# Performance work log

Measured on AMD Instinct MI355X. Metric: run time of the kernel, lower is better.

The kernel has to match this reference:

```python
import jax, jax.numpy as jnp
import numpy as np

N = 32768   # 'a' nodes
K = 8       # incoming edges per node (regular graph)
K2 = K // 2
E = N * K   # edges, stored as reverse pairs (2i, 2i+1)
D = 300     # hid_dim
H = 4       # attention heads
DEPTH = 3


def _build_graph():
    i = np.arange(N)
    src = np.empty(E, np.int64)
    mail = np.empty((N, K), np.int64)
    for d in range(1, K2 + 1):
        base = 2 * (i * K2 + (d - 1))
        src[base] = i                 # edge i -> (i+d)%N
        src[base + 1] = (i + d) % N   # reverse edge (i+d)%N -> i
        # incoming edges of node v: ((v-d)->v) and ((v+d)->v)
        mail[:, 2 * (d - 1)] = 2 * (((i - d) % N) * K2 + (d - 1))
        mail[:, 2 * (d - 1) + 1] = 2 * (i * K2 + (d - 1)) + 1
    return src, mail


def setup_inputs() -> dict:
    key = jax.random.key(0)
    ks = jax.random.split(key, 12)
    s = 1.0 / np.sqrt(D)
    src, mail = _build_graph()
    return {
        'f': jax.random.normal(ks[0], (N, D), jnp.float32),
        'x': jax.random.normal(ks[1], (E, D), jnp.float32),
        'mail_idx': jnp.asarray(mail),
        'src_idx': jnp.asarray(src),
        'Wq': jax.random.normal(ks[2], (D, D), jnp.float32) * s,
        'bq': jnp.zeros((D,), jnp.float32),
        'Wk': jax.random.normal(ks[3], (D, D), jnp.float32) * s,
        'bk': jnp.zeros((D,), jnp.float32),
        'Wv': jax.random.normal(ks[4], (D, D), jnp.float32) * s,
        'bv': jnp.zeros((D,), jnp.float32),
        'Wo': jax.random.normal(ks[5], (D, D), jnp.float32) * s,
        'bo': jnp.zeros((D,), jnp.float32),
        'Wmp': jax.random.normal(ks[6], (DEPTH - 1, D, D), jnp.float32) * s,
        'bmp': jnp.zeros((DEPTH - 1, D), jnp.float32),
        'Wlast': jax.random.normal(ks[7], (3 * D, D), jnp.float32) * s,
        'blast': jnp.zeros((D,), jnp.float32),
    }


def _mha(q_in, k_in, v_in, Wq, bq, Wk, bk, Wv, bv, Wo, bo):
    # q_in: [N,1,D], k_in/v_in: [N,K,D]  (per-node neighborhood attention)
    dk = D // H
    q = (q_in @ Wq + bq).reshape(N, 1, H, dk).transpose(0, 2, 1, 3)
    k = (k_in @ Wk + bk).reshape(N, -1, H, dk).transpose(0, 2, 1, 3)
    v = (v_in @ Wv + bv).reshape(N, -1, H, dk).transpose(0, 2, 1, 3)
    scores = jnp.einsum('nhqd,nhkd->nhqk', q, k) / jnp.sqrt(jnp.float32(dk))
    p = jax.nn.softmax(scores, axis=-1)
    o = jnp.einsum('nhqk,nhkd->nhqd', p, v).transpose(0, 2, 1, 3).reshape(N, 1, D)
    return o @ Wo + bo


def reference(f, x, mail_idx, src_idx, Wq, bq, Wk, bk, Wv, bv, Wo, bo,
              Wmp, bmp, Wlast, blast):
    rev = jnp.arange(E) ^ 1  # reverse_edge: swap within consecutive pairs
    f_h = f              # init_node: f_h = f.clone()
    h = x                # init_edge: h = x.clone()
    for i in range(DEPTH - 1):
        mail = h[mail_idx]                    # copy_e mailbox [N,K,D]
        feat = f_h[:, None, :]                # [N,1,D]
        # add_attn: attn(feat, mail, mail + feat)
        f_h = _mha(feat, mail, mail + feat,
                   Wq, bq, Wk, bk, Wv, bv, Wo, bo)[:, 0, :]
        rev_h = h[rev]                        # paired reverse-edge feature
        m = f_h[src_idx] - rev_h              # del_reverse_message
        h = jax.nn.relu(x + m @ Wmp[i] + bmp[i])  # update_edge
    # final node update: Linear(cat([sum(mailbox h), f_h, f]))
    mail_sum = jnp.sum(h[mail_idx], axis=1)   # [N,D]
    f_final = jnp.concatenate([mail_sum, f_h, f], axis=1) @ Wlast + blast
    return f_final
```

## Files before the change

### kernel.cpp

```cpp
#include <hip/hip_runtime.h>

typedef unsigned short u16;
typedef unsigned int u32;
typedef __bf16 bf16x8 __attribute__((ext_vector_type(8)));
typedef float f32x4 __attribute__((ext_vector_type(4)));

#define N_NODES 32768
#define E_EDGES 262144
#define BQ_U16 26240
#define S75 0.11547005383792515f

__device__ __forceinline__ float b2f(u16 u) {
    union { u32 u; float f; } x; x.u = ((u32)u) << 16; return x.f;
}
__device__ __forceinline__ u16 f2b(float f) {
    union { float f; u32 u; } x; x.f = f;
    u32 r = x.u + 0x7FFF + ((x.u >> 16) & 1);
    return (u16)(r >> 16);
}
__device__ __forceinline__ u32 bsub2(u32 a, u32 b) {
    float lo = b2f((u16)(a & 0xFFFF)) - b2f((u16)(b & 0xFFFF));
    float hi = b2f((u16)(a >> 16))    - b2f((u16)(b >> 16));
    return (u32)f2b(lo) | ((u32)f2b(hi) << 16);
}

#define GLOAD16(g, l) \
    __builtin_amdgcn_global_load_lds((const __attribute__((address_space(1))) u32*)(g), \
                                     (__attribute__((address_space(3))) u32*)(l), 16, 0, 0)

__global__ void convT_k(const float* __restrict__ src, int R, int C,
                        u16* __restrict__ dst, int KP_, long total) {
    long id = (long)blockIdx.x * blockDim.x + threadIdx.x;
    if (id >= total) return;
    int n = (int)(id / KP_), k = (int)(id % KP_);
    dst[id] = (k < R && n < C) ? f2b(src[(long)k * C + n]) : (u16)0;
}

__global__ void convTq_k(const float* __restrict__ src, u16* __restrict__ dst) {
    int id = blockIdx.x * 256 + threadIdx.x;
    if (id >= 4 * BQ_U16) return;
    int q = id / BQ_U16, rem = id % BQ_U16;
    int r = rem / 328, c = rem % 328;
    int n = q * 80 + r;
    dst[id] = (c < 300 && n < 300) ? f2b(src[(long)c * 300 + n]) : (u16)0;
}

__global__ void wqkq_k(const float* __restrict__ Wq, const float* __restrict__ Wk,
                       u16* __restrict__ dst) {
    int id = blockIdx.x * 256 + threadIdx.x;
    if (id >= 16 * BQ_U16) return;
    int q = id / BQ_U16, rem = id % BQ_U16;
    int r = rem / 328, c = rem % 328;
    int h = q >> 2;
    int cc = (q & 3) * 80 + r;
    float acc = 0.f;
    if (c < 300 && cc < 300) {
        const float* wq = Wq + (long)c * 300 + 75 * h;
        const float* wk = Wk + (long)cc * 300 + 75 * h;
        for (int d = 0; d < 75; ++d) acc += wq[d] * wk[d];
        acc *= S75;
    }
    dst[id] = f2b(acc);
}

__global__ void bqk_k(const float* __restrict__ bq, const float* __restrict__ Wk,
                      float* __restrict__ dst) {
    int n = blockIdx.x * 256 + threadIdx.x;
    if (n >= 1280) return;
    int h = n / 320, cc = n % 320;
    float acc = 0.f;
    if (cc < 300) {
        const float* b = bq + 75 * h;
        const float* wk = Wk + (long)cc * 300 + 75 * h;
        for (int d = 0; d < 75; ++d) acc += b[d] * wk[d];
        acc *= S75;
    }
    dst[n] = acc;
}

__global__ void ucat_k(const float* __restrict__ Wv, const float* __restrict__ Wo,
                       u16* __restrict__ dst) {
    long id = (long)blockIdx.x * 256 + threadIdx.x;
    if (id >= 320L * 1600) return;
    int n = (int)(id / 1600), k = (int)(id % 1600);
    float acc = 0.f;
    if (n < 300) {
        if (k < 1280) {
            int h = k / 320, a = k % 320;
            if (a < 300) {
                const float* wv = Wv + (long)a * 300 + 75 * h;
                const float* wo = Wo + (long)(75 * h) * 300 + n;
                for (int d = 0; d < 75; ++d) acc += wv[d] * wo[(long)d * 300];
            }
        } else {
            int a = k - 1280;
            if (a < 300) {
                const float* wv = Wv + (long)a * 300;
                const float* wo = Wo + n;
                for (int d = 0; d < 300; ++d) acc += wv[d] * wo[(long)d * 300];
            }
        }
    }
    dst[id] = f2b(acc);
}

__global__ void bvo_k(const float* __restrict__ bv, const float* __restrict__ Wo,
                      const float* __restrict__ bo, float* __restrict__ dst) {
    int n = blockIdx.x * 256 + threadIdx.x;
    if (n >= 320) return;
    float acc = 0.f;
    if (n < 300) {
        for (int d = 0; d < 300; ++d) acc += bv[d] * Wo[(long)d * 300 + n];
        acc += bo[n];
    }
    dst[n] = acc;
}

__global__ void padconv_k(const float* __restrict__ src, int C,
                          u16* __restrict__ dst, int CP,
                          u16* __restrict__ dst2, int CP2, long total) {
    long id = (long)blockIdx.x * blockDim.x + threadIdx.x;
    if (id >= total) return;
    int cw = CP >> 3;
    long row = id / cw;
    int c8 = (int)(id % cw) * 8;
    u32 w[4];
    #pragma unroll
    for (int p = 0; p < 4; ++p) {
        int c0 = c8 + 2 * p, c1 = c0 + 1;
        u16 lo = (c0 < C) ? f2b(src[row * C + c0]) : (u16)0;
        u16 hi = (c1 < C) ? f2b(src[row * C + c1]) : (u16)0;
        w[p] = (u32)lo | ((u32)hi << 16);
    }
    u32* d = (u32*)(dst + row * CP + c8);
    d[0] = w[0]; d[1] = w[1]; d[2] = w[2]; d[3] = w[3];
    if (dst2) {
        u32* d2 = (u32*)(dst2 + row * CP2 + c8);
        d2[0] = w[0]; d2[1] = w[1]; d2[2] = w[2]; d2[3] = w[3];
    }
}

#define TCOMP(KB, APTR) do { \
    bf16x8 av_[2], bb_[5]; \
    _Pragma("unroll") for (int fr = 0; fr < 2; ++fr) \
        av_[fr] = *(const bf16x8*)&(APTR)[ar0 + fr * 512]; \
    _Pragma("unroll") for (int fc = 0; fc < 5; ++fc) \
        bb_[fc] = *(const bf16x8*)&Bs[br0 + fc * 5248 + (KB) * 32]; \
    __builtin_amdgcn_s_setprio(1); \
    _Pragma("unroll") for (int fr = 0; fr < 2; ++fr) \
        _Pragma("unroll") for (int fc = 0; fc < 5; ++fc) \
            acc[fr][fc] = __builtin_amdgcn_mfma_f32_16x16x32_bf16(bb_[fc], av_[fr], acc[fr][fc], 0, 0, 0); \
    __builtin_amdgcn_s_setprio(0); \
} while (0)

__global__ __launch_bounds__(256, 2) void qgemm_k(
    const u16* __restrict__ A, const u16* __restrict__ Bswz,
    const float* __restrict__ bias, u16* __restrict__ outB)
{
    __shared__ __attribute__((aligned(16))) u16 Bs[80 * 328];
    __shared__ __attribute__((aligned(16))) u16 As3[3][128 * 32];
    const int tid = threadIdx.x;
    const int wf = tid >> 6, lane = tid & 63;
    const int tl = lane & 15, thi = lane >> 4;
    const int bid = blockIdx.x;
    const int gid = (bid & 7) * ((int)gridDim.x >> 3) + (bid >> 3);
    const long m0 = (long)(gid >> 4) * 128;
    const int q = gid & 15;
    const int n0 = q * 80;
    const int wf_u = __builtin_amdgcn_readfirstlane(wf);
    const u16* Bsrc = Bswz + q * BQ_U16;

    #pragma unroll
    for (int i = 0; i < 13; ++i) {
        int t = i * 256 + tid;
        if (t < 3280)
            GLOAD16(Bsrc + (long)t * 8, &Bs[(i * 256 + wf_u * 64) * 8]);
    }
    const int r1 = tid >> 2;
    const int g1 = (tid & 3) ^ ((r1 >> 1) & 3);
    const u16* gA0 = A + (m0 + r1) * 320L + g1 * 8;
    const u16* gA1 = A + (m0 + 64 + r1) * 320L + g1 * 8;

#define ESTAGE(KB) { \
    GLOAD16(gA0 + (KB) * 32, &As3[(KB) % 3][wf_u * 512]); \
    GLOAD16(gA1 + (KB) * 32, &As3[(KB) % 3][2048 + wf_u * 512]); }

    ESTAGE(0); ESTAGE(1);

    f32x4 acc[2][5];
    #pragma unroll
    for (int i = 0; i < 2; ++i)
        #pragma unroll
        for (int j = 0; j < 5; ++j) acc[i][j] = (f32x4)(0.f);
    const int ar0 = (wf * 32 + tl) * 32 + (thi ^ ((tl >> 1) & 3)) * 8;
    const int br0 = tl * 328 + thi * 8;

#define ESTEP(KB, VN) { \
    asm volatile("s_waitcnt vmcnt(" #VN ")" ::: "memory"); \
    __builtin_amdgcn_s_barrier(); \
    __builtin_amdgcn_sched_barrier(0); \
    if ((KB) + 2 < 10) ESTAGE((KB) + 2); \
    TCOMP(KB, (&As3[(KB) % 3][0])); }

    ESTEP(0, 2) ESTEP(1, 2) ESTEP(2, 2) ESTEP(3, 2) ESTEP(4, 2)
    ESTEP(5, 2) ESTEP(6, 2) ESTEP(7, 2) ESTEP(8, 2) ESTEP(9, 0)
#undef ESTEP
#undef ESTAGE

    #pragma unroll
    for (int fr = 0; fr < 2; ++fr) {
        const long row = m0 + wf * 32 + fr * 16 + tl;
        #pragma unroll
        for (int fc = 0; fc < 5; ++fc) {
            const int c0 = n0 + fc * 16 + thi * 4;
            f32x4 v = acc[fr][fc];
            const float4 bs = *(const float4*)&bias[c0];
            v[0] += bs.x; v[1] += bs.y; v[2] += bs.z; v[3] += bs.w;
            uint2 p;
            p.x = (u32)f2b(v[0]) | ((u32)f2b(v[1]) << 16);
            p.y = (u32)f2b(v[2]) | ((u32)f2b(v[3]) << 16);
            *(uint2*)&outB[row * 1280 + c0] = p;
        }
    }
}

__global__ __launch_bounds__(256) void attn2_k(
    const u16* __restrict__ qg, const u16* __restrict__ hcur,
    const int* __restrict__ mail, u16* __restrict__ wideA)
{
    const int tid = threadIdx.x;
    const long n = (long)blockIdx.x * 4 + (tid >> 6);
    const int lane = tid & 63;
    const bool act = lane < 40;
    const int ll = act ? lane : 39;

    int idx[8];
    #pragma unroll
    for (int j = 0; j < 8; ++j) idx[j] = mail[n * 8 + j];
    uint4 hr[8];
    #pragma unroll
    for (int j = 0; j < 8; ++j)
        hr[j] = *(const uint4*)&hcur[(long)idx[j] * 320 + ll * 8];
    uint4 qv[4];
    #pragma unroll
    for (int h = 0; h < 4; ++h)
        qv[h] = *(const uint4*)&qg[n * 1280 + h * 320 + ll * 8];
    if (!act) {
        #pragma unroll
        for (int j = 0; j < 8; ++j) hr[j] = make_uint4(0, 0, 0, 0);
    }

    float qf[4][8];
    #pragma unroll
    for (int h = 0; h < 4; ++h) {
        const u32 w[4] = {qv[h].x, qv[h].y, qv[h].z, qv[h].w};
        #pragma unroll
        for (int p = 0; p < 4; ++p) {
            qf[h][2 * p]     = b2f((u16)(w[p] & 0xFFFF));
            qf[h][2 * p + 1] = b2f((u16)(w[p] >> 16));
        }
    }

    float s[4][8];
    #pragma unroll
    for (int j = 0; j < 8; ++j) {
        float hf[8];
        const u32 w[4] = {hr[j].x, hr[j].y, hr[j].z, hr[j].w};
        #pragma unroll
        for (int p = 0; p < 4; ++p) {
            hf[2 * p]     = b2f((u16)(w[p] & 0xFFFF));
            hf[2 * p + 1] = b2f((u16)(w[p] >> 16));
        }
        #pragma unroll
        for (int h = 0; h < 4; ++h) {
            float d = 0.f;
            #pragma unroll
            for (int m = 0; m < 8; ++m) d += qf[h][m] * hf[m];
            d += __shfl_xor(d, 32, 64);
            d += __shfl_xor(d, 16, 64);
            d += __shfl_xor(d, 8, 64);
            d += __shfl_xor(d, 4, 64);
            d += __shfl_xor(d, 2, 64);
            d += __shfl_xor(d, 1, 64);
            s[h][j] = d;
        }
    }

    float p_[4][8];
    #pragma unroll
    for (int h = 0; h < 4; ++h) {
        float mx = s[h][0];
        #pragma unroll
        for (int j = 1; j < 8; ++j) mx = fmaxf(mx, s[h][j]);
        float sum = 0.f;
        #pragma unroll
        for (int j = 0; j < 8; ++j) { p_[h][j] = __expf(s[h][j] - mx); sum += p_[h][j]; }
        const float inv = 1.f / sum;
        #pragma unroll
        for (int j = 0; j < 8; ++j) p_[h][j] *= inv;
    }

    float y[4][8];
    #pragma unroll
    for (int h = 0; h < 4; ++h)
        #pragma unroll
        for (int m = 0; m < 8; ++m) y[h][m] = 0.f;
    #pragma unroll
    for (int j = 0; j < 8; ++j) {
        float hf[8];
        const u32 w[4] = {hr[j].x, hr[j].y, hr[j].z, hr[j].w};
        #pragma unroll
        for (int p = 0; p < 4; ++p) {
            hf[2 * p]     = b2f((u16)(w[p] & 0xFFFF));
            hf[2 * p + 1] = b2f((u16)(w[p] >> 16));
        }
        #pragma unroll
        for (int h = 0; h < 4; ++h)
            #pragma unroll
            for (int m = 0; m < 8; ++m) y[h][m] += p_[h][j] * hf[m];
    }
    if (act) {
        #pragma unroll
        for (int h = 0; h < 4; ++h) {
            uint4 o;
            o.x = (u32)f2b(y[h][0]) | ((u32)f2b(y[h][1]) << 16);
            o.y = (u32)f2b(y[h][2]) | ((u32)f2b(y[h][3]) << 16);
            o.z = (u32)f2b(y[h][4]) | ((u32)f2b(y[h][5]) << 16);
            o.w = (u32)f2b(y[h][6]) | ((u32)f2b(y[h][7]) << 16);
            *(uint4*)&wideA[n * 1600 + h * 320 + lane * 8] = o;
        }
    }
}

__global__ __launch_bounds__(256, 2) void egemmmb_k(
    const u16* __restrict__ fhb, const u16* __restrict__ hcur,
    const u16* __restrict__ hx, const int* __restrict__ srcidx,
    const u16* __restrict__ Bswz, const float* __restrict__ bias,
    u16* __restrict__ outB)
{
    __shared__ __attribute__((aligned(16))) u16 Bs[80 * 328];
    __shared__ __attribute__((aligned(16))) u16 As2[2][128 * 32];
    const int tid = threadIdx.x;
    const int wf = tid >> 6, lane = tid & 63;
    const int tl = lane & 15, thi = lane >> 4;
    const int bid = blockIdx.x;
    const int gid = (bid & 7) * ((int)gridDim.x >> 3) + (bid >> 3);
    const long m0 = (long)(gid >> 2) * 128;
    const int q = gid & 3;
    const int n0 = q * 80;
    const int wf_u = __builtin_amdgcn_readfirstlane(wf);
    const u16* Bsrc = Bswz + q * BQ_U16;

    #pragma unroll
    for (int i = 0; i < 13; ++i) {
        int t = i * 256 + tid;
        if (t < 3280)
            GLOAD16(Bsrc + (long)t * 8, &Bs[(i * 256 + wf_u * 64) * 8]);
    }
    const int r1 = tid >> 2;
    const int g1 = (tid & 3) ^ ((r1 >> 1) & 3);
    const long e0 = m0 + r1, e1 = m0 + 64 + r1;
    const u16* pF0 = fhb + (long)srcidx[e0] * 320 + g1 * 8;
    const u16* pH0 = hcur + (e0 ^ 1) * 320 + g1 * 8;
    const u16* pF1 = fhb + (long)srcidx[e1] * 320 + g1 * 8;
    const u16* pH1 = hcur + (e1 ^ 1) * 320 + g1 * 8;

    uint4 Fa0, Ha0, Fa1, Ha1, Fb0, Hb0, Fb1, Hb1, Fc0, Hc0, Fc1, Hc1;

#define MLOAD(KB, F0, H0, F1, H1) { \
    F0 = *(const uint4*)(pF0 + (KB) * 32); H0 = *(const uint4*)(pH0 + (KB) * 32); \
    F1 = *(const uint4*)(pF1 + (KB) * 32); H1 = *(const uint4*)(pH1 + (KB) * 32); }

#define MWRITE(KB, F0, H0, F1, H1) { \
    u16* wb_ = &As2[(KB) & 1][0]; \
    uint4 o_; \
    o_.x = bsub2(F0.x, H0.x); o_.y = bsub2(F0.y, H0.y); \
    o_.z = bsub2(F0.z, H0.z); o_.w = bsub2(F0.w, H0.w); \
    *(uint4*)&wb_[tid * 8] = o_; \
    o_.x = bsub2(F1.x, H1.x); o_.y = bsub2(F1.y, H1.y); \
    o_.z = bsub2(F1.z, H1.z); o_.w = bsub2(F1.w, H1.w); \
    *(uint4*)&wb_[(tid + 256) * 8] = o_; }

    MLOAD(0, Fa0, Ha0, Fa1, Ha1);
    MLOAD(1, Fb0, Hb0, Fb1, Hb1);
    MLOAD(2, Fc0, Hc0, Fc1, Hc1);
    asm volatile("s_waitcnt vmcnt(8)" ::: "memory");
    MWRITE(0, Fa0, Ha0, Fa1, Ha1);

    f32x4 acc[2][5];
    #pragma unroll
    for (int i = 0; i < 2; ++i)
        #pragma unroll
        for (int j = 0; j < 5; ++j) acc[i][j] = (f32x4)(0.f);
    const int ar0 = (wf * 32 + tl) * 32 + (thi ^ ((tl >> 1) & 3)) * 8;
    const int br0 = tl * 328 + thi * 8;

#define MSTEP(KB, VN, LF0, LH0, LF1, LH1, SF0, SH0, SF1, SH1) { \
    if ((KB) + 3 < 10) MLOAD((KB) + 3, LF0, LH0, LF1, LH1); \
    asm volatile("s_waitcnt vmcnt(" #VN ")" ::: "memory"); \
    asm volatile("s_waitcnt lgkmcnt(0)" ::: "memory"); \
    __builtin_amdgcn_s_barrier(); \
    __builtin_amdgcn_sched_barrier(0); \
    if ((KB) + 1 < 10) MWRITE((KB) + 1, SF0, SH0, SF1, SH1); \
    TCOMP(KB, (&As2[(KB) & 1][0])); }

    MSTEP(0, 8, Fa0, Ha0, Fa1, Ha1, Fb0, Hb0, Fb1, Hb1)
    MSTEP(1, 8, Fb0, Hb0, Fb1, Hb1, Fc0, Hc0, Fc1, Hc1)
    MSTEP(2, 8, Fc0, Hc0, Fc1, Hc1, Fa0, Ha0, Fa1, Ha1)
    MSTEP(3, 8, Fa0, Ha0, Fa1, Ha1, Fb0, Hb0, Fb1, Hb1)
    MSTEP(4, 8, Fb0, Hb0, Fb1, Hb1, Fc0, Hc0, Fc1, Hc1)
    MSTEP(5, 8, Fc0, Hc0, Fc1, Hc1, Fa0, Ha0, Fa1, Ha1)
    MSTEP(6, 8, Fa0, Ha0, Fa1, Ha1, Fb0, Hb0, Fb1, Hb1)
    MSTEP(7, 4, Fb0, Hb0, Fb1, Hb1, Fc0, Hc0, Fc1, Hc1)
    MSTEP(8, 0, Fc0, Hc0, Fc1, Hc1, Fa0, Ha0, Fa1, Ha1)
    MSTEP(9, 0, Fa0, Ha0, Fa1, Ha1, Fb0, Hb0, Fb1, Hb1)
#undef MSTEP
#undef MLOAD
#undef MWRITE

    #pragma unroll
    for (int fr = 0; fr < 2; ++fr) {
        const long row = m0 + wf * 32 + fr * 16 + tl;
        #pragma unroll
        for (int fc = 0; fc < 5; ++fc) {
            const int c0 = n0 + fc * 16 + thi * 4;
            f32x4 v = acc[fr][fc];
            if (bias && c0 < 300) {
                const float4 bs = *(const float4*)&bias[c0];
                v[0] += bs.x; v[1] += bs.y; v[2] += bs.z; v[3] += bs.w;
            }
            {
                const ushort4 xv = *(const ushort4*)&hx[row * 320 + c0];
                v[0] += b2f(xv.x); v[1] += b2f(xv.y); v[2] += b2f(xv.z); v[3] += b2f(xv.w);
            }
            v[0] = fmaxf(v[0], 0.f); v[1] = fmaxf(v[1], 0.f);
            v[2] = fmaxf(v[2], 0.f); v[3] = fmaxf(v[3], 0.f);
            uint2 p;
            p.x = (u32)f2b(v[0]) | ((u32)f2b(v[1]) << 16);
            p.y = (u32)f2b(v[2]) | ((u32)f2b(v[3]) << 16);
            *(uint2*)&outB[row * 320 + c0] = p;
        }
    }
}

#define LOADB(bq, kt1) { const long ko_ = (long)(kt1) << 6; \
    _Pragma("unroll") for (int fc = 0; fc < 5; ++fc) \
      _Pragma("unroll") for (int ks = 0; ks < 2; ++ks) \
        bq[fc][ks] = *(const bf16x8*)(gBw + (long)fc * 16 * KP + ko_ + ks * 32); }

#define READA(lkt) { \
    _Pragma("unroll") for (int fr = 0; fr < 4; ++fr) \
      _Pragma("unroll") for (int ks = 0; ks < 2; ++ks) \
        a[fr][ks] = *(const bf16x8*)&As[(fr * 16 + tl) * 320 + ((((lkt) * 8 + ks * 4 + thi) ^ sx) * 8)]; }

#define DOMFMA(bq) { _Pragma("unroll") for (int fr = 0; fr < 4; ++fr) \
    _Pragma("unroll") for (int fc = 0; fc < 5; ++fc) \
      _Pragma("unroll") for (int ks = 0; ks < 2; ++ks) \
        acc[fr][fc] = __builtin_amdgcn_mfma_f32_16x16x32_bf16(bq[fc][ks], a[fr][ks], acc[fr][fc], 0, 0, 0); }

template<int KP>
__global__ __launch_bounds__(256, 2) void gemm_k(
    const u16* __restrict__ A,
    const u16* __restrict__ BT,
    const float* __restrict__ bias,
    float* __restrict__ outF, int ostride, int ocols,
    u16* __restrict__ outB1, long strideB1,
    u16* __restrict__ outB2, long strideB2)
{
    __shared__ u16 As[64 * 320];
    const int tid = threadIdx.x;
    const int w = tid >> 6, lane = tid & 63;
    const int tl = lane & 15, thi = lane >> 4;
    const int sx = tl & 7;
    const long m0 = (long)blockIdx.x * 64;
    const int w_u = __builtin_amdgcn_readfirstlane(w);

    const u16* gBw = BT + ((long)(w * 80 + tl)) * KP + thi * 8;

    f32x4 acc[4][5];
    #pragma unroll
    for (int i = 0; i < 4; ++i)
        #pragma unroll
        for (int j = 0; j < 5; ++j) acc[i][j] = (f32x4)(0.f);

    constexpr int NCH = KP / 320;
    constexpr int NST = KP >> 6;
    bf16x8 bA[5][2], bB[5][2], a[4][2];

    #pragma unroll
    for (int kb = 0; kb < NCH; ++kb) {
        if (kb) __syncthreads();
        #pragma unroll
        for (int i = 0; i < 10; ++i) {
            const int c = i * 256 + w_u * 64 + lane;
            const int r = c / 40, s = c - r * 40;
            GLOAD16(A + (m0 + r) * (long)KP + kb * 320 + ((s ^ (r & 7)) * 8),
                    &As[(i * 256 + w_u * 64) * 8]);
        }
        if (kb == 0) LOADB(bA, 0);
        __syncthreads();
        #pragma unroll
        for (int lkt = 0; lkt < 5; ++lkt) {
            const int kt = kb * 5 + lkt;
            if (kt + 1 < NST) {
                if (kt & 1) { LOADB(bA, kt + 1); } else { LOADB(bB, kt + 1); }
            }
            READA(lkt);
            if (kt & 1) { DOMFMA(bB); } else { DOMFMA(bA); }
        }
    }

    #pragma unroll
    for (int fr = 0; fr < 4; ++fr) {
        const long row = m0 + fr * 16 + tl;
        #pragma unroll
        for (int fc = 0; fc < 5; ++fc) {
            const int c0 = w * 80 + fc * 16 + thi * 4;
            f32x4 v = acc[fr][fc];
            if (bias && c0 < 300) {
                const float4 bs = *(const float4*)&bias[c0];
                v[0] += bs.x; v[1] += bs.y; v[2] += bs.z; v[3] += bs.w;
            }
            if (outF && c0 < ocols)
                *(float4*)&outF[row * (long)ostride + c0] = make_float4(v[0], v[1], v[2], v[3]);
            if (outB1 || outB2) {
                uint2 p;
                p.x = (u32)f2b(v[0]) | ((u32)f2b(v[1]) << 16);
                p.y = (u32)f2b(v[2]) | ((u32)f2b(v[3]) << 16);
                if (outB1) *(uint2*)&outB1[row * strideB1 + c0] = p;
                if (outB2) *(uint2*)&outB2[row * strideB2 + c0] = p;
            }
        }
    }
}

__global__ __launch_bounds__(256) void concat_k(
    const u16* __restrict__ hb, const u16* __restrict__ fhb,
    const float* __restrict__ f, const int* __restrict__ mail,
    u16* __restrict__ Acat)
{
    const long n = blockIdx.x;
    int m[8];
    #pragma unroll
    for (int j = 0; j < 8; ++j) m[j] = mail[n * 8 + j];
    for (int c = threadIdx.x; c < 960; c += 256) {
        float v;
        if (c < 300) {
            float s = 0.f;
            #pragma unroll
            for (int j = 0; j < 8; ++j) s += b2f(hb[(long)m[j] * 320 + c]);
            v = s;
        } else if (c < 600) v = b2f(fhb[n * 320 + (c - 300)]);
        else if (c < 900) v = f[n * 300 + (c - 600)];
        else v = 0.f;
        Acat[n * 960 + c] = f2b(v);
    }
}

extern "C" void kernel_launch(void* const* d_in, const int* in_sizes, int n_in,
                              void* d_out, int out_size, void* d_ws, size_t ws_size,
                              hipStream_t stream)
{
    const int N = N_NODES, E = E_EDGES;
    const float* f    = (const float*)d_in[0];
    const float* x    = (const float*)d_in[1];
    const int*   mail = (const int*)d_in[2];
    const int*   srcx = (const int*)d_in[3];
    const float* Wq = (const float*)d_in[4];   const float* bq = (const float*)d_in[5];
    const float* Wk = (const float*)d_in[6];
    const float* Wv = (const float*)d_in[8];   const float* bv = (const float*)d_in[9];
    const float* Wo = (const float*)d_in[10];  const float* bo = (const float*)d_in[11];
    const float* Wmp = (const float*)d_in[12]; const float* bmp = (const float*)d_in[13];
    const float* Wlast = (const float*)d_in[14]; const float* blast = (const float*)d_in[15];
    float* out = (float*)d_out;

    char* ws = (char*)d_ws;
    size_t off = 0;
    auto alloc = [&](size_t b) -> void* {
        void* p = ws + off; off += (b + 255) & ~(size_t)255; return p;
    };
    u16* hb    = (u16*)alloc((size_t)E * 320 * 2);
    u16* hb2   = (u16*)alloc((size_t)E * 320 * 2);
    u16* qgb   = (u16*)alloc((size_t)N * 1280 * 2);
    u16* wideA = (u16*)alloc((size_t)N * 1600 * 2);
    u16* fhb   = (u16*)alloc((size_t)N * 320 * 2);
    u16* Acat  = (u16*)alloc((size_t)N * 960 * 2);
    u16* WqkS  = (u16*)alloc((size_t)16 * BQ_U16 * 2);
    u16* Wm0S  = (u16*)alloc((size_t)4 * BQ_U16 * 2);
    u16* Wm1S  = (u16*)alloc((size_t)4 * BQ_U16 * 2);
    u16* UcatT = (u16*)alloc((size_t)320 * 1600 * 2);
    u16* WcatB = (u16*)alloc((size_t)960 * 320 * 2);
    float* bqkF = (float*)alloc(1280 * 4);
    float* bvoF = (float*)alloc(320 * 4);

    {
        wqkq_k<<<(16 * BQ_U16 + 255) / 256, 256, 0, stream>>>(Wq, Wk, WqkS);
        bqk_k<<<5, 256, 0, stream>>>(bq, Wk, bqkF);
        ucat_k<<<(int)((320L * 1600 + 255) / 256), 256, 0, stream>>>(Wv, Wo, UcatT);
        bvo_k<<<2, 256, 0, stream>>>(bv, Wo, bo, bvoF);
        int blks = (4 * BQ_U16 + 255) / 256;
        convTq_k<<<blks, 256, 0, stream>>>(Wmp, Wm0S);
        convTq_k<<<blks, 256, 0, stream>>>(Wmp + 90000, Wm1S);
        long totc = (long)320 * 960;
        convT_k<<<(int)((totc + 255) / 256), 256, 0, stream>>>(Wlast, 900, 300, WcatB, 960, totc);
    }
    {
        long totE = (long)E * 40;
        padconv_k<<<(int)((totE + 255) / 256), 256, 0, stream>>>(x, 300, hb, 320, nullptr, 0, totE);
        long totN = (long)N * 40;
        padconv_k<<<(int)((totN + 255) / 256), 256, 0, stream>>>(f, 300, fhb, 320, wideA + 1280, 1600, totN);
    }

    const int GQG = (N / 128) * 16;
    const int GE  = (E / 128) * 4;

    for (int it = 0; it < 2; ++it) {
        const u16* WmS = it ? Wm1S : Wm0S;
        const float* bmpi = bmp + it * 300;
        const u16* hcur = it ? hb2 : hb;
        u16* hnxt = it ? hb : hb2;
        qgemm_k<<<GQG, 256, 0, stream>>>(fhb, WqkS, bqkF, qgb);
        attn2_k<<<N / 4, 256, 0, stream>>>(qgb, hcur, mail, wideA);
        gemm_k<1600><<<N / 64, 256, 0, stream>>>(wideA, UcatT, bvoF,
                                                 nullptr, 0, 0, fhb, 320, wideA + 1280, 1600);
        egemmmb_k<<<GE, 256, 0, stream>>>(fhb, hcur, hb, srcx, WmS, bmpi, hnxt);
    }

    concat_k<<<N, 256, 0, stream>>>(hb, fhb, f, mail, Acat);
    gemm_k<960><<<N / 64, 256, 0, stream>>>(Acat, WcatB, blast, out, 300, 300,
                                            nullptr, 0, nullptr, 0);
}
```

Before: 1.385 ms.

## Restructure edge GEMM into 160-column tiles with per-wave private A buffers

The edge message GEMM now uses 512-thread blocks, each covering 128 edges by 160 output columns (two column halves instead of four quarters). This halves how many times each edge's gathered f_h[src] minus h[rev] row is loaded and subtracted. Each wave builds its own 16-row A slice in a private LDS buffer with K=64 steps, so the per-step block barriers go away. Bs grows to about 104KB of LDS and there are 10 accumulators per wave, which risks lower occupancy and higher register pressure.

```diff
diff --git a/kernel.cpp b/kernel.cpp
--- a/kernel.cpp
+++ b/kernel.cpp
@@ -8,6 +8,7 @@
 #define N_NODES 32768
 #define E_EDGES 262144
 #define BQ_U16 26240
+#define BH_U16 53248
 #define S75 0.11547005383792515f
 
 __device__ __forceinline__ float b2f(u16 u) {
@@ -43,6 +44,19 @@
     int r = rem / 328, c = rem % 328;
     int n = q * 80 + r;
     dst[id] = (c < 300 && n < 300) ? f2b(src[(long)c * 300 + n]) : (u16)0;
+}
+
+__global__ void convTh_k(const float* __restrict__ src, u16* __restrict__ dst) {
+    int id = blockIdx.x * 256 + threadIdx.x;
+    if (id >= 2 * BH_U16) return;
+    int h = id / BH_U16, rem = id % BH_U16;
+    u16 v = 0;
+    if (rem < 160 * 328) {
+        int r = rem / 328, c = rem % 328;
+        int n = h * 160 + r;
+        v = (c < 300 && n < 300) ? f2b(src[(long)c * 300 + n]) : (u16)0;
+    }
+    dst[id] = v;
 }
 
 __global__ void wqkq_k(const float* __restrict__ Wq, const float* __restrict__ Wk,
@@ -332,114 +346,109 @@
     }
 }
 
-__global__ __launch_bounds__(256, 2) void egemmmb_k(
+__global__ __launch_bounds__(512, 2) void egemmmb_k(
     const u16* __restrict__ fhb, const u16* __restrict__ hcur,
     const u16* __restrict__ hx, const int* __restrict__ srcidx,
     const u16* __restrict__ Bswz, const float* __restrict__ bias,
     u16* __restrict__ outB)
 {
-    __shared__ __attribute__((aligned(16))) u16 Bs[80 * 328];
-    __shared__ __attribute__((aligned(16))) u16 As2[2][128 * 32];
+    __shared__ __attribute__((aligned(16))) u16 Bs[BH_U16];
+    __shared__ __attribute__((aligned(16))) u16 As[8 * 2 * 1152];
     const int tid = threadIdx.x;
     const int wf = tid >> 6, lane = tid & 63;
     const int tl = lane & 15, thi = lane >> 4;
     const int bid = blockIdx.x;
     const int gid = (bid & 7) * ((int)gridDim.x >> 3) + (bid >> 3);
-    const long m0 = (long)(gid >> 2) * 128;
-    const int q = gid & 3;
-    const int n0 = q * 80;
+    const long m0 = (long)(gid >> 1) * 128;
+    const int n0 = (gid & 1) * 160;
     const int wf_u = __builtin_amdgcn_readfirstlane(wf);
-    const u16* Bsrc = Bswz + q * BQ_U16;
-
-    #pragma unroll
-    for (int i = 0; i < 13; ++i) {
-        int t = i * 256 + tid;
-        if (t < 3280)
-            GLOAD16(Bsrc + (long)t * 8, &Bs[(i * 256 + wf_u * 64) * 8]);
-    }
-    const int r1 = tid >> 2;
-    const int g1 = (tid & 3) ^ ((r1 >> 1) & 3);
-    const long e0 = m0 + r1, e1 = m0 + 64 + r1;
-    const u16* pF0 = fhb + (long)srcidx[e0] * 320 + g1 * 8;
-    const u16* pH0 = hcur + (e0 ^ 1) * 320 + g1 * 8;
-    const u16* pF1 = fhb + (long)srcidx[e1] * 320 + g1 * 8;
-    const u16* pH1 = hcur + (e1 ^ 1) * 320 + g1 * 8;
+    const u16* Bsrc = Bswz + (gid & 1) * BH_U16;
+
+    #pragma unroll
+    for (int i = 0; i < 13; ++i)
+        GLOAD16(Bsrc + (long)(i * 512 + tid) * 8, &Bs[(i * 512 + wf_u * 64) * 8]);
+    __builtin_amdgcn_sched_barrier(0);
+
+    const int rw = lane >> 3;
+    const int up = lane & 7;
+    const long e0 = m0 + wf * 16 + rw;
+    const long e1 = e0 + 8;
+    const u16* pF0 = fhb + (long)srcidx[e0] * 320 + up * 8;
+    const u16* pH0 = hcur + (e0 ^ 1) * 320 + up * 8;
+    const u16* pF1 = fhb + (long)srcidx[e1] * 320 + up * 8;
+    const u16* pH1 = hcur + (e1 ^ 1) * 320 + up * 8;
+    u16* Aw = &As[wf * 2304];
+    const int wi0 = rw * 72 + up * 8;
+    const int wi1 = wi0 + 576;
 
     uint4 Fa0, Ha0, Fa1, Ha1, Fb0, Hb0, Fb1, Hb1, Fc0, Hc0, Fc1, Hc1;
 
-#define MLOAD(KB, F0, H0, F1, H1) { \
-    F0 = *(const uint4*)(pF0 + (KB) * 32); H0 = *(const uint4*)(pH0 + (KB) * 32); \
-    F1 = *(const uint4*)(pF1 + (KB) * 32); H1 = *(const uint4*)(pH1 + (KB) * 32); }
-
-#define MWRITE(KB, F0, H0, F1, H1) { \
-    u16* wb_ = &As2[(KB) & 1][0]; \
-    uint4 o_; \
+#define MLOADG(KB, F0, H0, F1, H1) { \
+    F0 = *(const uint4*)(pF0 + (KB) * 64); H0 = *(const uint4*)(pH0 + (KB) * 64); \
+    F1 = *(const uint4*)(pF1 + (KB) * 64); H1 = *(const uint4*)(pH1 + (KB) * 64); }
+
+#define MWRITEG(KB, F0, H0, F1, H1) { \
+    u16* wb_ = Aw + ((KB) & 1) * 1152; uint4 o_; \
     o_.x = bsub2(F0.x, H0.x); o_.y = bsub2(F0.y, H0.y); \
     o_.z = bsub2(F0.z, H0.z); o_.w = bsub2(F0.w, H0.w); \
-    *(uint4*)&wb_[tid * 8] = o_; \
+    *(uint4*)&wb_[wi0] = o_; \
     o_.x = bsub2(F1.x, H1.x); o_.y = bsub2(F1.y, H1.y); \
     o_.z = bsub2(F1.z, H1.z); o_.w = bsub2(F1.w, H1.w); \
-    *(uint4*)&wb_[(tid + 256) * 8] = o_; }
-
-    MLOAD(0, Fa0, Ha0, Fa1, Ha1);
-    MLOAD(1, Fb0, Hb0, Fb1, Hb1);
-    MLOAD(2, Fc0, Hc0, Fc1, Hc1);
+    *(uint4*)&wb_[wi1] = o_; }
+
+    f32x4 acc[10];
+    #pragma unroll
+    for (int j = 0; j < 10; ++j) acc[j] = (f32x4)(0.f);
+
+#define GCOMP(KB) { \
+    const u16* ab_ = Aw + ((KB) & 1) * 1152; \
+    bf16x8 a0_ = *(const bf16x8*)&ab_[tl * 72 + thi * 8]; \
+    bf16x8 a1_ = *(const bf16x8*)&ab_[tl * 72 + thi * 8 + 32]; \
+    __builtin_amdgcn_s_setprio(1); \
+    _Pragma("unroll") for (int fc = 0; fc < 10; ++fc) { \
+        const u16* br_ = &Bs[(fc * 16 + tl) * 328 + thi * 8 + (KB) * 64]; \
+        bf16x8 b0_ = *(const bf16x8*)&br_[0]; \
+        acc[fc] = __builtin_amdgcn_mfma_f32_16x16x32_bf16(b0_, a0_, acc[fc], 0, 0, 0); \
+        bf16x8 b1_ = *(const bf16x8*)&br_[32]; \
+        acc[fc] = __builtin_amdgcn_mfma_f32_16x16x32_bf16(b1_, a1_, acc[fc], 0, 0, 0); } \
+    __builtin_amdgcn_s_setprio(0); }
+
+    MLOADG(0, Fa0, Ha0, Fa1, Ha1);
+    MLOADG(1, Fb0, Hb0, Fb1, Hb1);
+    __builtin_amdgcn_sched_barrier(0);
     asm volatile("s_waitcnt vmcnt(8)" ::: "memory");
-    MWRITE(0, Fa0, Ha0, Fa1, Ha1);
-
-    f32x4 acc[2][5];
-    #pragma unroll
-    for (int i = 0; i < 2; ++i)
-        #pragma unroll
-        for (int j = 0; j < 5; ++j) acc[i][j] = (f32x4)(0.f);
-    const int ar0 = (wf * 32 + tl) * 32 + (thi ^ ((tl >> 1) & 3)) * 8;
-    const int br0 = tl * 328 + thi * 8;
-
-#define MSTEP(KB, VN, LF0, LH0, LF1, LH1, SF0, SH0, SF1, SH1) { \
-    if ((KB) + 3 < 10) MLOAD((KB) + 3, LF0, LH0, LF1, LH1); \
-    asm volatile("s_waitcnt vmcnt(" #VN ")" ::: "memory"); \
-    asm volatile("s_waitcnt lgkmcnt(0)" ::: "memory"); \
-    __builtin_amdgcn_s_barrier(); \
-    __builtin_amdgcn_sched_barrier(0); \
-    if ((KB) + 1 < 10) MWRITE((KB) + 1, SF0, SH0, SF1, SH1); \
-    TCOMP(KB, (&As2[(KB) & 1][0])); }
-
-    MSTEP(0, 8, Fa0, Ha0, Fa1, Ha1, Fb0, Hb0, Fb1, Hb1)
-    MSTEP(1, 8, Fb0, Hb0, Fb1, Hb1, Fc0, Hc0, Fc1, Hc1)
-    MSTEP(2, 8, Fc0, Hc0, Fc1, Hc1, Fa0, Ha0, Fa1, Ha1)
-    MSTEP(3, 8, Fa0, Ha0, Fa1, Ha1, Fb0, Hb0, Fb1, Hb1)
-    MSTEP(4, 8, Fb0, Hb0, Fb1, Hb1, Fc0, Hc0, Fc1, Hc1)
-    MSTEP(5, 8, Fc0, Hc0, Fc1, Hc1, Fa0, Ha0, Fa1, Ha1)
-    MSTEP(6, 8, Fa0, Ha0, Fa1, Ha1, Fb0, Hb0, Fb1, Hb1)
-    MSTEP(7, 4, Fb0, Hb0, Fb1, Hb1, Fc0, Hc0, Fc1, Hc1)
-    MSTEP(8, 0, Fc0, Hc0, Fc1, Hc1, Fa0, Ha0, Fa1, Ha1)
-    MSTEP(9, 0, Fa0, Ha0, Fa1, Ha1, Fb0, Hb0, Fb1, Hb1)
-#undef MSTEP
-#undef MLOAD
-#undef MWRITE
-
-    #pragma unroll
-    for (int fr = 0; fr < 2; ++fr) {
-        const long row = m0 + wf * 32 + fr * 16 + tl;
-        #pragma unroll
-        for (int fc = 0; fc < 5; ++fc) {
-            const int c0 = n0 + fc * 16 + thi * 4;
-            f32x4 v = acc[fr][fc];
-            if (bias && c0 < 300) {
-                const float4 bs = *(const float4*)&bias[c0];
-                v[0] += bs.x; v[1] += bs.y; v[2] += bs.z; v[3] += bs.w;
-            }
-            {
-                const ushort4 xv = *(const ushort4*)&hx[row * 320 + c0];
-                v[0] += b2f(xv.x); v[1] += b2f(xv.y); v[2] += b2f(xv.z); v[3] += b2f(xv.w);
-            }
-            v[0] = fmaxf(v[0], 0.f); v[1] = fmaxf(v[1], 0.f);
-            v[2] = fmaxf(v[2], 0.f); v[3] = fmaxf(v[3], 0.f);
-            uint2 p;
-            p.x = (u32)f2b(v[0]) | ((u32)f2b(v[1]) << 16);
-            p.y = (u32)f2b(v[2]) | ((u32)f2b(v[3]) << 16);
-            *(uint2*)&outB[row * 320 + c0] = p;
-        }
+    __builtin_amdgcn_s_barrier();
+    __builtin_amdgcn_sched_barrier(0);
+    MWRITEG(0, Fa0, Ha0, Fa1, Ha1);
+
+    MLOADG(2, Fc0, Hc0, Fc1, Hc1); GCOMP(0); MWRITEG(1, Fb0, Hb0, Fb1, Hb1);
+    MLOADG(3, Fa0, Ha0, Fa1, Ha1); GCOMP(1); MWRITEG(2, Fc0, Hc0, Fc1, Hc1);
+    MLOADG(4, Fb0, Hb0, Fb1, Hb1); GCOMP(2); MWRITEG(3, Fa0, Ha0, Fa1, Ha1);
+    GCOMP(3); MWRITEG(4, Fb0, Hb0, Fb1, Hb1);
+    GCOMP(4);
+#undef MLOADG
+#undef MWRITEG
+#undef GCOMP
+
+    const long row = m0 + wf * 16 + tl;
+    #pragma unroll
+    for (int fc = 0; fc < 10; ++fc) {
+        const int c0 = n0 + fc * 16 + thi * 4;
+        f32x4 v = acc[fc];
+        if (c0 < 300) {
+            const float4 bs = *(const float4*)&bias[c0];
+            v[0] += bs.x; v[1] += bs.y; v[2] += bs.z; v[3] += bs.w;
+        }
+        {
+            const ushort4 xv = *(const ushort4*)&hx[row * 320 + c0];
+            v[0] += b2f(xv.x); v[1] += b2f(xv.y); v[2] += b2f(xv.z); v[3] += b2f(xv.w);
+        }
+        v[0] = fmaxf(v[0], 0.f); v[1] = fmaxf(v[1], 0.f);
+        v[2] = fmaxf(v[2], 0.f); v[3] = fmaxf(v[3], 0.f);
+        uint2 p;
+        p.x = (u32)f2b(v[0]) | ((u32)f2b(v[1]) << 16);
+        p.y = (u32)f2b(v[2]) | ((u32)f2b(v[3]) << 16);
+        *(uint2*)&outB[row * 320 + c0] = p;
     }
 }
 
@@ -586,8 +595,8 @@
     u16* fhb   = (u16*)alloc((size_t)N * 320 * 2);
     u16* Acat  = (u16*)alloc((size_t)N * 960 * 2);
     u16* WqkS  = (u16*)alloc((size_t)16 * BQ_U16 * 2);
-    u16* Wm0S  = (u16*)alloc((size_t)4 * BQ_U16 * 2);
-    u16* Wm1S  = (u16*)alloc((size_t)4 * BQ_U16 * 2);
+    u16* Wm0S  = (u16*)alloc((size_t)2 * BH_U16 * 2);
+    u16* Wm1S  = (u16*)alloc((size_t)2 * BH_U16 * 2);
     u16* UcatT = (u16*)alloc((size_t)320 * 1600 * 2);
     u16* WcatB = (u16*)alloc((size_t)960 * 320 * 2);
     float* bqkF = (float*)alloc(1280 * 4);
@@ -598,9 +607,9 @@
         bqk_k<<<5, 256, 0, stream>>>(bq, Wk, bqkF);
         ucat_k<<<(int)((320L * 1600 + 255) / 256), 256, 0, stream>>>(Wv, Wo, UcatT);
         bvo_k<<<2, 256, 0, stream>>>(bv, Wo, bo, bvoF);
-        int blks = (4 * BQ_U16 + 255) / 256;
-        convTq_k<<<blks, 256, 0, stream>>>(Wmp, Wm0S);
-        convTq_k<<<blks, 256, 0, stream>>>(Wmp + 90000, Wm1S);
+        int blksh = (2 * BH_U16 + 255) / 256;
+        convTh_k<<<blksh, 256, 0, stream>>>(Wmp, Wm0S);
+        convTh_k<<<blksh, 256, 0, stream>>>(Wmp + 90000, Wm1S);
         long totc = (long)320 * 960;
         convT_k<<<(int)((totc + 255) / 256), 256, 0, stream>>>(Wlast, 900, 300, WcatB, 960, totc);
     }
@@ -612,7 +621,7 @@
     }
 
     const int GQG = (N / 128) * 16;
-    const int GE  = (E / 128) * 4;
+    const int GE2 = (E / 128) * 2;
 
     for (int it = 0; it < 2; ++it) {
         const u16* WmS = it ? Wm1S : Wm0S;
@@ -623,7 +632,7 @@
         attn2_k<<<N / 4, 256, 0, stream>>>(qgb, hcur, mail, wideA);
         gemm_k<1600><<<N / 64, 256, 0, stream>>>(wideA, UcatT, bvoF,
                                                  nullptr, 0, 0, fhb, 320, wideA + 1280, 1600);
-        egemmmb_k<<<GE, 256, 0, stream>>>(fhb, hcur, hb, srcx, WmS, bmpi, hnxt);
+        egemmmb_k<<<GE2, 512, 0, stream>>>(fhb, hcur, hb, srcx, WmS, bmpi, hnxt);
     }
 
     concat_k<<<N, 256, 0, stream>>>(hb, fhb, f, mail, Acat);
```

After: 1.297 ms. 6.3% less time.

## Feed gathered edge message directly into MFMA registers, halve edge tile

Applied to the files above, without the earlier changes.

The edge GEMM now builds the A operand (f_h[src] - h[rev]) in registers and passes it straight to MFMA. This drops the LDS staging buffer and the per-k-step barriers. The M tile per block shrinks from 128 to 64 rows, which doubles the grid and halves the accumulators per wave. The price is reloading the 80x320 weight slice into LDS twice as often across blocks, with fewer MFMAs to amortise each B read from LDS.

```diff
diff --git a/kernel.cpp b/kernel.cpp
--- a/kernel.cpp
+++ b/kernel.cpp
@@ -339,13 +339,12 @@
     u16* __restrict__ outB)
 {
     __shared__ __attribute__((aligned(16))) u16 Bs[80 * 328];
-    __shared__ __attribute__((aligned(16))) u16 As2[2][128 * 32];
     const int tid = threadIdx.x;
     const int wf = tid >> 6, lane = tid & 63;
     const int tl = lane & 15, thi = lane >> 4;
     const int bid = blockIdx.x;
     const int gid = (bid & 7) * ((int)gridDim.x >> 3) + (bid >> 3);
-    const long m0 = (long)(gid >> 2) * 128;
+    const long m0 = (long)(gid >> 2) * 64;
     const int q = gid & 3;
     const int n0 = q * 80;
     const int wf_u = __builtin_amdgcn_readfirstlane(wf);
@@ -357,89 +356,74 @@
         if (t < 3280)
             GLOAD16(Bsrc + (long)t * 8, &Bs[(i * 256 + wf_u * 64) * 8]);
     }
-    const int r1 = tid >> 2;
-    const int g1 = (tid & 3) ^ ((r1 >> 1) & 3);
-    const long e0 = m0 + r1, e1 = m0 + 64 + r1;
-    const u16* pF0 = fhb + (long)srcidx[e0] * 320 + g1 * 8;
-    const u16* pH0 = hcur + (e0 ^ 1) * 320 + g1 * 8;
-    const u16* pF1 = fhb + (long)srcidx[e1] * 320 + g1 * 8;
-    const u16* pH1 = hcur + (e1 ^ 1) * 320 + g1 * 8;
-
-    uint4 Fa0, Ha0, Fa1, Ha1, Fb0, Hb0, Fb1, Hb1, Fc0, Hc0, Fc1, Hc1;
-
-#define MLOAD(KB, F0, H0, F1, H1) { \
-    F0 = *(const uint4*)(pF0 + (KB) * 32); H0 = *(const uint4*)(pH0 + (KB) * 32); \
-    F1 = *(const uint4*)(pF1 + (KB) * 32); H1 = *(const uint4*)(pH1 + (KB) * 32); }
-
-#define MWRITE(KB, F0, H0, F1, H1) { \
-    u16* wb_ = &As2[(KB) & 1][0]; \
-    uint4 o_; \
-    o_.x = bsub2(F0.x, H0.x); o_.y = bsub2(F0.y, H0.y); \
-    o_.z = bsub2(F0.z, H0.z); o_.w = bsub2(F0.w, H0.w); \
-    *(uint4*)&wb_[tid * 8] = o_; \
-    o_.x = bsub2(F1.x, H1.x); o_.y = bsub2(F1.y, H1.y); \
-    o_.z = bsub2(F1.z, H1.z); o_.w = bsub2(F1.w, H1.w); \
-    *(uint4*)&wb_[(tid + 256) * 8] = o_; }
-
-    MLOAD(0, Fa0, Ha0, Fa1, Ha1);
-    MLOAD(1, Fb0, Hb0, Fb1, Hb1);
-    MLOAD(2, Fc0, Hc0, Fc1, Hc1);
+    __builtin_amdgcn_sched_barrier(0);
+
+    const long e = m0 + wf * 16 + tl;
+    const u16* pF = fhb + (long)srcidx[e] * 320 + thi * 8;
+    const u16* pH = hcur + (e ^ 1) * 320 + thi * 8;
+
+    uint4 Fa0, Fa1, Ha0, Ha1, Fb0, Fb1, Hb0, Hb1, Fc0, Fc1, Hc0, Hc1;
+
+#define MLD(KB, F0, F1, H0, H1) { \
+    F0 = *(const uint4*)(pF + (KB) * 64);      F1 = *(const uint4*)(pF + (KB) * 64 + 32); \
+    H0 = *(const uint4*)(pH + (KB) * 64);      H1 = *(const uint4*)(pH + (KB) * 64 + 32); }
+
+    MLD(0, Fa0, Fa1, Ha0, Ha1);
+    MLD(1, Fb0, Fb1, Hb0, Hb1);
+    __builtin_amdgcn_sched_barrier(0);
     asm volatile("s_waitcnt vmcnt(8)" ::: "memory");
-    MWRITE(0, Fa0, Ha0, Fa1, Ha1);
-
-    f32x4 acc[2][5];
-    #pragma unroll
-    for (int i = 0; i < 2; ++i)
-        #pragma unroll
-        for (int j = 0; j < 5; ++j) acc[i][j] = (f32x4)(0.f);
-    const int ar0 = (wf * 32 + tl) * 32 + (thi ^ ((tl >> 1) & 3)) * 8;
+    __builtin_amdgcn_s_barrier();
+    __builtin_amdgcn_sched_barrier(0);
+
+    f32x4 acc[5];
+    #pragma unroll
+    for (int j = 0; j < 5; ++j) acc[j] = (f32x4)(0.f);
     const int br0 = tl * 328 + thi * 8;
 
-#define MSTEP(KB, VN, LF0, LH0, LF1, LH1, SF0, SH0, SF1, SH1) { \
-    if ((KB) + 3 < 10) MLOAD((KB) + 3, LF0, LH0, LF1, LH1); \
-    asm volatile("s_waitcnt vmcnt(" #VN ")" ::: "memory"); \
-    asm volatile("s_waitcnt lgkmcnt(0)" ::: "memory"); \
-    __builtin_amdgcn_s_barrier(); \
-    __builtin_amdgcn_sched_barrier(0); \
-    if ((KB) + 1 < 10) MWRITE((KB) + 1, SF0, SH0, SF1, SH1); \
-    TCOMP(KB, (&As2[(KB) & 1][0])); }
-
-    MSTEP(0, 8, Fa0, Ha0, Fa1, Ha1, Fb0, Hb0, Fb1, Hb1)
-    MSTEP(1, 8, Fb0, Hb0, Fb1, Hb1, Fc0, Hc0, Fc1, Hc1)
-    MSTEP(2, 8, Fc0, Hc0, Fc1, Hc1, Fa0, Ha0, Fa1, Ha1)
-    MSTEP(3, 8, Fa0, Ha0, Fa1, Ha1, Fb0, Hb0, Fb1, Hb1)
-    MSTEP(4, 8, Fb0, Hb0, Fb1, Hb1, Fc0, Hc0, Fc1, Hc1)
-    MSTEP(5, 8, Fc0, Hc0, Fc1, Hc1, Fa0, Ha0, Fa1, Ha1)
-    MSTEP(6, 8, Fa0, Ha0, Fa1, Ha1, Fb0, Hb0, Fb1, Hb1)
-    MSTEP(7, 4, Fb0, Hb0, Fb1, Hb1, Fc0, Hc0, Fc1, Hc1)
-    MSTEP(8, 0, Fc0, Hc0, Fc1, Hc1, Fa0, Ha0, Fa1, Ha1)
-    MSTEP(9, 0, Fa0, Ha0, Fa1, Ha1, Fb0, Hb0, Fb1, Hb1)
-#undef MSTEP
-#undef MLOAD
-#undef MWRITE
-
-    #pragma unroll
-    for (int fr = 0; fr < 2; ++fr) {
-        const long row = m0 + wf * 32 + fr * 16 + tl;
-        #pragma unroll
-        for (int fc = 0; fc < 5; ++fc) {
-            const int c0 = n0 + fc * 16 + thi * 4;
-            f32x4 v = acc[fr][fc];
-            if (bias && c0 < 300) {
-                const float4 bs = *(const float4*)&bias[c0];
-                v[0] += bs.x; v[1] += bs.y; v[2] += bs.z; v[3] += bs.w;
-            }
-            {
-                const ushort4 xv = *(const ushort4*)&hx[row * 320 + c0];
-                v[0] += b2f(xv.x); v[1] += b2f(xv.y); v[2] += b2f(xv.z); v[3] += b2f(xv.w);
-            }
-            v[0] = fmaxf(v[0], 0.f); v[1] = fmaxf(v[1], 0.f);
-            v[2] = fmaxf(v[2], 0.f); v[3] = fmaxf(v[3], 0.f);
-            uint2 p;
-            p.x = (u32)f2b(v[0]) | ((u32)f2b(v[1]) << 16);
-            p.y = (u32)f2b(v[2]) | ((u32)f2b(v[3]) << 16);
-            *(uint2*)&outB[row * 320 + c0] = p;
-        }
+#define GC(KB, F0, F1, H0, H1) { \
+    uint4 o0_, o1_; \
+    o0_.x = bsub2(F0.x, H0.x); o0_.y = bsub2(F0.y, H0.y); \
+    o0_.z = bsub2(F0.z, H0.z); o0_.w = bsub2(F0.w, H0.w); \
+    o1_.x = bsub2(F1.x, H1.x); o1_.y = bsub2(F1.y, H1.y); \
+    o1_.z = bsub2(F1.z, H1.z); o1_.w = bsub2(F1.w, H1.w); \
+    bf16x8 av0_ = *(const bf16x8*)&o0_; \
+    bf16x8 av1_ = *(const bf16x8*)&o1_; \
+    __builtin_amdgcn_s_setprio(1); \
+    _Pragma("unroll") for (int fc = 0; fc < 5; ++fc) { \
+        const u16* br_ = &Bs[br0 + fc * 5248 + (KB) * 64]; \
+        bf16x8 b0_ = *(const bf16x8*)&br_[0]; \
+        acc[fc] = __builtin_amdgcn_mfma_f32_16x16x32_bf16(b0_, av0_, acc[fc], 0, 0, 0); \
+        bf16x8 b1_ = *(const bf16x8*)&br_[32]; \
+        acc[fc] = __builtin_amdgcn_mfma_f32_16x16x32_bf16(b1_, av1_, acc[fc], 0, 0, 0); } \
+    __builtin_amdgcn_s_setprio(0); }
+
+    MLD(2, Fc0, Fc1, Hc0, Hc1); GC(0, Fa0, Fa1, Ha0, Ha1);
+    MLD(3, Fa0, Fa1, Ha0, Ha1); GC(1, Fb0, Fb1, Hb0, Hb1);
+    MLD(4, Fb0, Fb1, Hb0, Hb1); GC(2, Fc0, Fc1, Hc0, Hc1);
+    GC(3, Fa0, Fa1, Ha0, Ha1);
+    GC(4, Fb0, Fb1, Hb0, Hb1);
+#undef GC
+#undef MLD
+
+    const long row = m0 + wf * 16 + tl;
+    #pragma unroll
+    for (int fc = 0; fc < 5; ++fc) {
+        const int c0 = n0 + fc * 16 + thi * 4;
+        f32x4 v = acc[fc];
+        if (c0 < 300) {
+            const float4 bs = *(const float4*)&bias[c0];
+            v[0] += bs.x; v[1] += bs.y; v[2] += bs.z; v[3] += bs.w;
+        }
+        {
+            const ushort4 xv = *(const ushort4*)&hx[row * 320 + c0];
+            v[0] += b2f(xv.x); v[1] += b2f(xv.y); v[2] += b2f(xv.z); v[3] += b2f(xv.w);
+        }
+        v[0] = fmaxf(v[0], 0.f); v[1] = fmaxf(v[1], 0.f);
+        v[2] = fmaxf(v[2], 0.f); v[3] = fmaxf(v[3], 0.f);
+        uint2 p;
+        p.x = (u32)f2b(v[0]) | ((u32)f2b(v[1]) << 16);
+        p.y = (u32)f2b(v[2]) | ((u32)f2b(v[3]) << 16);
+        *(uint2*)&outB[row * 320 + c0] = p;
     }
 }
 
@@ -612,7 +596,7 @@
     }
 
     const int GQG = (N / 128) * 16;
-    const int GE  = (E / 128) * 4;
+    const int GE4 = (E / 64) * 4;
 
     for (int it = 0; it < 2; ++it) {
         const u16* WmS = it ? Wm1S : Wm0S;
@@ -623,7 +607,7 @@
         attn2_k<<<N / 4, 256, 0, stream>>>(qgb, hcur, mail, wideA);
         gemm_k<1600><<<N / 64, 256, 0, stream>>>(wideA, UcatT, bvoF,
                                                  nullptr, 0, 0, fhb, 320, wideA + 1280, 1600);
-        egemmmb_k<<<GE, 256, 0, stream>>>(fhb, hcur, hb, srcx, WmS, bmpi, hnxt);
+        egemmmb_k<<<GE4, 256, 0, stream>>>(fhb, hcur, hb, srcx, WmS, bmpi, hnxt);
     }
 
     concat_k<<<N, 256, 0, stream>>>(hb, fhb, f, mail, Acat);
```

Measured after the change: 1.384 ms. Within noise of the previous version (-0.1%).
